# Optimization experiments

Hardware: AMD Instinct MI355X
Metric: run time of the kernel (lower is better)

Reference implementation:

```python
import jax, jax.numpy as jnp
import numpy as np
import math

B, D, L = 32, 128, 512
NH = 8
DK = D // NH  # 16
DV = D // NH  # 16


def setup_inputs() -> dict:
    key = jax.random.key(0)
    kx, kq, kk, kv, ko = jax.random.split(key, 5)
    # xavier_normal std for [B, Dk, D] slabs: gain*sqrt(2/(fan_in+fan_out)) with fan over last two dims
    std_qkv = math.sqrt(2.0 / (DK + D))
    std_o = math.sqrt(2.0 / (DV * NH + D))
    x = jax.random.normal(kx, (B, D, L), dtype=jnp.float32)
    Wqs = jax.random.normal(kq, (NH, B, DK, D), dtype=jnp.float32) * std_qkv
    Wks = jax.random.normal(kk, (NH, B, DK, D), dtype=jnp.float32) * std_qkv
    Wvs = jax.random.normal(kv, (NH, B, DV, D), dtype=jnp.float32) * std_qkv
    Wo = jax.random.normal(ko, (B, DV * NH, D), dtype=jnp.float32) * std_o
    return {"x": x, "Wqs": Wqs, "Wks": Wks, "Wvs": Wvs, "Wo": Wo}


def reference(x, Wqs, Wks, Wvs, Wo):
    # x: [B, D, L]; Wqs/Wks: [NH, B, DK, D]; Wvs: [NH, B, DV, D]; Wo: [B, DV*NH, D]
    nh, b, dk, d = Wqs.shape
    l = x.shape[-1]
    inv_sqrt_dk = 1.0 / math.sqrt(dk)
    Q = jnp.einsum('nbkd,bdl->nbkl', Wqs, x)  # [NH, B, DK, L]
    K = jnp.einsum('nbkd,bdl->nbkl', Wks, x)  # [NH, B, DK, L]
    V = jnp.einsum('nbvd,bdl->nbvl', Wvs, x)  # [NH, B, DV, L]
    # scores[n,b,l,m] = sum_k Q[n,b,k,l]*K[n,b,k,m]; softmax over l (torch dim=1 of [B,L,L])
    scores = jnp.einsum('nbkl,nbkm->nblm', Q, K) * inv_sqrt_dk
    S = jax.nn.softmax(scores, axis=2)
    heads = jnp.einsum('nbvl,nblm->nbvm', V, S)  # [NH, B, DV, L]
    # .pop() in the original reverses head order before concatenation
    heads = heads[::-1]
    head = heads.transpose(1, 0, 2, 3).reshape(b, nh * heads.shape[2], l)  # [B, NH*DV, L]
    out = jnp.einsum('bod,bdl->bol', Wo, head)  # [B, D, L]
    return out
```

## Files before the change

kernel.cpp:

```cpp
#include <hip/hip_runtime.h>
#include <hip/hip_bf16.h>
#include <math.h>

#define B_   32
#define D_   128
#define L_   512
#define NH_  8
#define DK_  16

#define QKS  24
#define VST  520

#define LOG2E 1.4426950408889634f
#define QSC   (0.25f * LOG2E)
#define SH2   (-11.541560327111707f)

typedef _Float16 h2 __attribute__((ext_vector_type(2)));
typedef _Float16 h4 __attribute__((ext_vector_type(4)));
typedef _Float16 h8 __attribute__((ext_vector_type(8)));
typedef __attribute__((ext_vector_type(4)))  float f32x4;
typedef __attribute__((ext_vector_type(16))) float f32x16;
typedef unsigned int u32x2 __attribute__((ext_vector_type(2)));
typedef unsigned int u32x4 __attribute__((ext_vector_type(4)));

__device__ __forceinline__ unsigned int cvt_pk_u(float a, float b) {
    return __builtin_bit_cast(unsigned int, __builtin_amdgcn_cvt_pkrtz(a, b));
}

#define MFMA_K32(a, b, c) __builtin_amdgcn_mfma_f32_16x16x32_f16((a), (b), (c), 0, 0, 0)
#define MFMA_32(a, b, c)  __builtin_amdgcn_mfma_f32_32x32x16_f16((a), (b), (c), 0, 0, 0)

__global__ __launch_bounds__(256) void xcast(
    const float* __restrict__ x,
    _Float16* __restrict__ xt)
{
    __shared__ _Float16 T[64][130];
    const int lt = blockIdx.x;
    const int b  = blockIdx.y;
    const int t  = threadIdx.x;
    const float* xb = x + (size_t)b * D_ * L_;
    _Float16* xtb = xt + (size_t)b * L_ * D_;

    #pragma unroll
    for (int i = t; i < 64 * 128; i += 256) {
        const int l = i & 63, d = i >> 6;
        T[l][d] = (_Float16)xb[(size_t)d * L_ + lt * 64 + l];
    }
    __syncthreads();
    #pragma unroll
    for (int i = t; i < 64 * 128; i += 256) {
        const int d = i & 127, l = i >> 7;
        xtb[(size_t)(lt * 64 + l) * D_ + d] = T[l][d];
    }
}

__global__ __launch_bounds__(512, 2) void attn_mfma(
    const _Float16* __restrict__ xt,
    const float* __restrict__ Wq,
    const float* __restrict__ Wk,
    const float* __restrict__ Wv,
    _Float16* __restrict__ Ht)
{
    __shared__ __attribute__((aligned(16))) _Float16 Qh[512 * QKS];
    __shared__ __attribute__((aligned(16))) _Float16 Kh[512 * QKS];
    __shared__ __attribute__((aligned(16))) _Float16 Vs[32 * VST];

    const int nb = blockIdx.x;
    const int n  = nb >> 5;
    const int b  = nb & 31;
    const int t  = threadIdx.x;
    const int wv = t >> 6;
    const int ln = t & 63;
    const int l16 = ln & 15;
    const int g4  = ln >> 4;
    const int lm  = ln & 31;
    const int hi  = ln >> 5;

    const _Float16* xtb = xt + (size_t)b * L_ * D_;
    const size_t woff = (size_t)(n * B_ + b) * DK_ * D_;
    const float* pWq = Wq + woff;
    const float* pWk = Wk + woff;
    const float* pWv = Wv + woff;

    {
        const h8 ones8 = {(_Float16)1.f,(_Float16)1.f,(_Float16)1.f,(_Float16)1.f,
                          (_Float16)1.f,(_Float16)1.f,(_Float16)1.f,(_Float16)1.f};
        #pragma unroll
        for (int i = 0; i < 2; ++i) {
            const int c = t + i * 512;
            const int row = 16 + (c >> 6), cc = (c & 63) * 8;
            *(h8*)&Vs[row * VST + cc] = ones8;
        }
    }

    f32x4 Qa[4], Ka[4], Va[4];
    #pragma unroll
    for (int lt = 0; lt < 4; ++lt) {
        Qa[lt] = (f32x4){0.f,0.f,0.f,0.f};
        Ka[lt] = (f32x4){0.f,0.f,0.f,0.f};
        Va[lt] = (f32x4){0.f,0.f,0.f,0.f};
    }

    #pragma unroll
    for (int ks = 0; ks < 4; ++ks) {
        const int d0 = ks * 32 + g4 * 8;
        const float* aq = pWq + l16 * D_ + d0;
        const float* ak = pWk + l16 * D_ + d0;
        const float* av = pWv + l16 * D_ + d0;
        const float4 q0 = *(const float4*)aq, q1 = *(const float4*)(aq + 4);
        const float4 k0 = *(const float4*)ak, k1 = *(const float4*)(ak + 4);
        const float4 v0 = *(const float4*)av, v1 = *(const float4*)(av + 4);
        h8 Aq, Ak, Av;
        Aq[0]=(_Float16)q0.x; Aq[1]=(_Float16)q0.y; Aq[2]=(_Float16)q0.z; Aq[3]=(_Float16)q0.w;
        Aq[4]=(_Float16)q1.x; Aq[5]=(_Float16)q1.y; Aq[6]=(_Float16)q1.z; Aq[7]=(_Float16)q1.w;
        Ak[0]=(_Float16)k0.x; Ak[1]=(_Float16)k0.y; Ak[2]=(_Float16)k0.z; Ak[3]=(_Float16)k0.w;
        Ak[4]=(_Float16)k1.x; Ak[5]=(_Float16)k1.y; Ak[6]=(_Float16)k1.z; Ak[7]=(_Float16)k1.w;
        Av[0]=(_Float16)v0.x; Av[1]=(_Float16)v0.y; Av[2]=(_Float16)v0.z; Av[3]=(_Float16)v0.w;
        Av[4]=(_Float16)v1.x; Av[5]=(_Float16)v1.y; Av[6]=(_Float16)v1.z; Av[7]=(_Float16)v1.w;
        #pragma unroll
        for (int lt = 0; lt < 4; ++lt) {
            const int l = wv * 64 + lt * 16 + l16;
            const h8 Bx = *(const h8*)&xtb[(size_t)l * D_ + d0];
            Qa[lt] = MFMA_K32(Aq, Bx, Qa[lt]);
            Ka[lt] = MFMA_K32(Ak, Bx, Ka[lt]);
            Va[lt] = MFMA_K32(Av, Bx, Va[lt]);
        }
    }

    #pragma unroll
    for (int lt = 0; lt < 4; ++lt) {
        const int l = wv * 64 + lt * 16 + l16;
        h4 qv, kv;
        #pragma unroll
        for (int r = 0; r < 4; ++r) {
            qv[r] = (_Float16)(Qa[lt][r] * QSC);
            kv[r] = (_Float16)Ka[lt][r];
            Vs[(g4 * 4 + r) * VST + l] = (_Float16)Va[lt][r];
        }
        *(h4*)&Qh[l * QKS + g4 * 4] = qv;
        *(h4*)&Kh[l * QKS + g4 * 4] = kv;
    }
    __syncthreads();

    const int m0 = wv * 64;
    const h8 Bk0 = *(const h8*)&Kh[(m0 + lm) * QKS + 8 * hi];
    const h8 Bk1 = *(const h8*)&Kh[(m0 + 32 + lm) * QKS + 8 * hi];

    f32x16 shiftacc, pv0, pv1;
    #pragma unroll
    for (int i = 0; i < 16; ++i) { shiftacc[i] = SH2; pv0[i] = 0.f; pv1[i] = 0.f; }

    #pragma unroll 2
    for (int t32 = 0; t32 < 16; ++t32) {
        const int lb = t32 * 32;
        const h8 Aq2 = *(const h8*)&Qh[(lb + lm) * QKS + 8 * hi];
        const h8 Bv1 = *(const h8*)&Vs[lm * VST + lb + 8 * hi];
        const h8 Bv2 = *(const h8*)&Vs[lm * VST + lb + 16 + 8 * hi];

        const f32x16 sc0 = MFMA_32(Aq2, Bk0, shiftacc);
        const f32x16 sc1 = MFMA_32(Aq2, Bk1, shiftacc);

        float pA[16], pB[16];
        #pragma unroll
        for (int r = 0; r < 16; ++r) pA[r] = __builtin_amdgcn_exp2f(sc0[r]);
        #pragma unroll
        for (int r = 0; r < 16; ++r) pB[r] = __builtin_amdgcn_exp2f(sc1[r]);

        const unsigned int a0 = cvt_pk_u(pA[0],  pA[1]);
        const unsigned int a1 = cvt_pk_u(pA[2],  pA[3]);
        const unsigned int a2 = cvt_pk_u(pA[4],  pA[5]);
        const unsigned int a3 = cvt_pk_u(pA[6],  pA[7]);
        const unsigned int a4 = cvt_pk_u(pA[8],  pA[9]);
        const unsigned int a5 = cvt_pk_u(pA[10], pA[11]);
        const unsigned int a6 = cvt_pk_u(pA[12], pA[13]);
        const unsigned int a7 = cvt_pk_u(pA[14], pA[15]);
        const unsigned int b0 = cvt_pk_u(pB[0],  pB[1]);
        const unsigned int b1 = cvt_pk_u(pB[2],  pB[3]);
        const unsigned int b2 = cvt_pk_u(pB[4],  pB[5]);
        const unsigned int b3 = cvt_pk_u(pB[6],  pB[7]);
        const unsigned int b4 = cvt_pk_u(pB[8],  pB[9]);
        const unsigned int b5 = cvt_pk_u(pB[10], pB[11]);
        const unsigned int b6 = cvt_pk_u(pB[12], pB[13]);
        const unsigned int b7 = cvt_pk_u(pB[14], pB[15]);

        const u32x2 sA02 = __builtin_amdgcn_permlane32_swap(a0, a2, false, false);
        const u32x2 sA13 = __builtin_amdgcn_permlane32_swap(a1, a3, false, false);
        const u32x2 sA46 = __builtin_amdgcn_permlane32_swap(a4, a6, false, false);
        const u32x2 sA57 = __builtin_amdgcn_permlane32_swap(a5, a7, false, false);
        const u32x2 sB02 = __builtin_amdgcn_permlane32_swap(b0, b2, false, false);
        const u32x2 sB13 = __builtin_amdgcn_permlane32_swap(b1, b3, false, false);
        const u32x2 sB46 = __builtin_amdgcn_permlane32_swap(b4, b6, false, false);
        const u32x2 sB57 = __builtin_amdgcn_permlane32_swap(b5, b7, false, false);
        const h8 A1m0 = __builtin_bit_cast(h8, (u32x4){sA02.x, sA13.x, sA02.y, sA13.y});
        const h8 A2m0 = __builtin_bit_cast(h8, (u32x4){sA46.x, sA57.x, sA46.y, sA57.y});
        const h8 A1m1 = __builtin_bit_cast(h8, (u32x4){sB02.x, sB13.x, sB02.y, sB13.y});
        const h8 A2m1 = __builtin_bit_cast(h8, (u32x4){sB46.x, sB57.x, sB46.y, sB57.y});

        pv0 = MFMA_32(A1m0, Bv1, pv0);
        pv0 = MFMA_32(A2m0, Bv2, pv0);
        pv1 = MFMA_32(A1m1, Bv1, pv1);
        pv1 = MFMA_32(A2m1, Bv2, pv1);
    }

    const int kk = (NH_ - 1 - n) * 16 + l16;
    const int zlane = 16 + 32 * hi;
    _Float16* Hb = Ht + (size_t)b * 512 * 128;
    #pragma unroll
    for (int r = 0; r < 16; ++r) {
        const int mrow = (r & 3) + 8 * (r >> 2) + 4 * hi;
        const float zr0 = __shfl(pv0[r], zlane);
        const float zr1 = __shfl(pv1[r], zlane);
        const float rz0 = __builtin_amdgcn_rcpf(zr0);
        const float rz1 = __builtin_amdgcn_rcpf(zr1);
        if (lm < 16) {
            Hb[(size_t)(m0 + mrow) * 128 + kk]      = (_Float16)(pv0[r] * rz0);
            Hb[(size_t)(m0 + 32 + mrow) * 128 + kk] = (_Float16)(pv1[r] * rz1);
        }
    }
}

__global__ __launch_bounds__(512) void out_proj_mfma(
    const float* __restrict__ Wo,
    const _Float16* __restrict__ Ht,
    float* __restrict__ out)
{
    const int ct = blockIdx.x;
    const int b  = blockIdx.y;
    const int t  = threadIdx.x;
    const int wv = t >> 6;
    const int ln = t & 63;
    const int l16 = ln & 15;
    const int g4  = ln >> 4;

    const float* Wb = Wo + (size_t)b * D_ * D_;
    const _Float16* Hb = Ht + (size_t)b * 512 * 128;

    f32x4 acc[4];
    #pragma unroll
    for (int nt = 0; nt < 4; ++nt) acc[nt] = (f32x4){0.f,0.f,0.f,0.f};

    #pragma unroll
    for (int ks = 0; ks < 4; ++ks) {
        const int k0 = ks * 32 + g4 * 8;
        const float* ap = Wb + (size_t)(wv * 16 + l16) * D_ + k0;
        const float4 w0 = *(const float4*)ap, w1 = *(const float4*)(ap + 4);
        h8 Ah;
        Ah[0]=(_Float16)w0.x; Ah[1]=(_Float16)w0.y; Ah[2]=(_Float16)w0.z; Ah[3]=(_Float16)w0.w;
        Ah[4]=(_Float16)w1.x; Ah[5]=(_Float16)w1.y; Ah[6]=(_Float16)w1.z; Ah[7]=(_Float16)w1.w;
        #pragma unroll
        for (int nt = 0; nt < 4; ++nt) {
            const h8 Bh = *(const h8*)&Hb[(size_t)(ct * 64 + nt * 16 + l16) * 128 + k0];
            acc[nt] = MFMA_K32(Ah, Bh, acc[nt]);
        }
    }

    float* ob = out + (size_t)b * D_ * L_;
    #pragma unroll
    for (int nt = 0; nt < 4; ++nt) {
        #pragma unroll
        for (int r = 0; r < 4; ++r) {
            ob[(size_t)(wv * 16 + g4 * 4 + r) * L_ + ct * 64 + nt * 16 + l16] = acc[nt][r];
        }
    }
}

extern "C" void kernel_launch(void* const* d_in, const int* in_sizes, int n_in,
                              void* d_out, int out_size, void* d_ws, size_t ws_size,
                              hipStream_t stream)
{
    const float* x  = (const float*)d_in[0];
    const float* Wq = (const float*)d_in[1];
    const float* Wk = (const float*)d_in[2];
    const float* Wv = (const float*)d_in[3];
    const float* Wo = (const float*)d_in[4];
    float* out = (float*)d_out;

    _Float16* Ht = (_Float16*)d_ws;
    _Float16* xt = Ht + (size_t)B_ * 512 * 128;

    xcast<<<dim3(8, B_), dim3(256), 0, stream>>>(x, xt);
    attn_mfma<<<dim3(NH_ * B_), dim3(512), 0, stream>>>(xt, Wq, Wk, Wv, Ht);
    out_proj_mfma<<<dim3(8, B_), dim3(512), 0, stream>>>(Wo, Ht, out);
}
```

Baseline: 40.26 us.

## Fuse x transpose-cast into attention kernel via LDS staging

Removes the separate xcast kernel and instead has each attention block load fp32 x slices, convert to fp16 and transpose into an LDS tile per K-step before the QKV MFMAs. This eliminates one kernel launch and the global round trip of the fp16 transposed x. In exchange, each of the 8 head blocks per batch re-reads and re-converts the same x, adds two barriers per K-step, and raises LDS usage (about 40KB more), which may hurt the two-blocks-per-CU occupancy target.

```diff
diff --git a/kernel.cpp b/kernel.cpp
--- a/kernel.cpp
+++ b/kernel.cpp
@@ -10,6 +10,7 @@
 
 #define QKS  24
 #define VST  520
+#define XST  40
 
 #define LOG2E 1.4426950408889634f
 #define QSC   (0.25f * LOG2E)
@@ -30,37 +31,14 @@
 #define MFMA_K32(a, b, c) __builtin_amdgcn_mfma_f32_16x16x32_f16((a), (b), (c), 0, 0, 0)
 #define MFMA_32(a, b, c)  __builtin_amdgcn_mfma_f32_32x32x16_f16((a), (b), (c), 0, 0, 0)
 
-__global__ __launch_bounds__(256) void xcast(
+__global__ __launch_bounds__(512, 2) void attn_mfma(
     const float* __restrict__ x,
-    _Float16* __restrict__ xt)
-{
-    __shared__ _Float16 T[64][130];
-    const int lt = blockIdx.x;
-    const int b  = blockIdx.y;
-    const int t  = threadIdx.x;
-    const float* xb = x + (size_t)b * D_ * L_;
-    _Float16* xtb = xt + (size_t)b * L_ * D_;
-
-    #pragma unroll
-    for (int i = t; i < 64 * 128; i += 256) {
-        const int l = i & 63, d = i >> 6;
-        T[l][d] = (_Float16)xb[(size_t)d * L_ + lt * 64 + l];
-    }
-    __syncthreads();
-    #pragma unroll
-    for (int i = t; i < 64 * 128; i += 256) {
-        const int d = i & 127, l = i >> 7;
-        xtb[(size_t)(lt * 64 + l) * D_ + d] = T[l][d];
-    }
-}
-
-__global__ __launch_bounds__(512, 2) void attn_mfma(
-    const _Float16* __restrict__ xt,
     const float* __restrict__ Wq,
     const float* __restrict__ Wk,
     const float* __restrict__ Wv,
     _Float16* __restrict__ Ht)
 {
+    __shared__ __attribute__((aligned(16))) _Float16 T32[512 * XST];
     __shared__ __attribute__((aligned(16))) _Float16 Qh[512 * QKS];
     __shared__ __attribute__((aligned(16))) _Float16 Kh[512 * QKS];
     __shared__ __attribute__((aligned(16))) _Float16 Vs[32 * VST];
@@ -76,7 +54,7 @@
     const int lm  = ln & 31;
     const int hi  = ln >> 5;
 
-    const _Float16* xtb = xt + (size_t)b * L_ * D_;
+    const float* xb = x + (size_t)b * D_ * L_;
     const size_t woff = (size_t)(n * B_ + b) * DK_ * D_;
     const float* pWq = Wq + woff;
     const float* pWk = Wk + woff;
@@ -93,6 +71,9 @@
         }
     }
 
+    const int sdd = (t >> 7) * 8;
+    const int sl0 = (t & 127) * 4;
+
     f32x4 Qa[4], Ka[4], Va[4];
     #pragma unroll
     for (int lt = 0; lt < 4; ++lt) {
@@ -101,30 +82,45 @@
         Va[lt] = (f32x4){0.f,0.f,0.f,0.f};
     }
 
-    #pragma unroll
     for (int ks = 0; ks < 4; ++ks) {
+        {
+            f32x4 xv[8];
+            #pragma unroll
+            for (int j = 0; j < 8; ++j)
+                xv[j] = *(const f32x4*)&xb[(size_t)(ks * 32 + sdd + j) * L_ + sl0];
+            #pragma unroll
+            for (int i = 0; i < 4; ++i) {
+                h8 w;
+                #pragma unroll
+                for (int j = 0; j < 8; ++j) w[j] = (_Float16)xv[j][i];
+                *(h8*)&T32[(sl0 + i) * XST + sdd] = w;
+            }
+        }
+        __syncthreads();
+
         const int d0 = ks * 32 + g4 * 8;
         const float* aq = pWq + l16 * D_ + d0;
         const float* ak = pWk + l16 * D_ + d0;
         const float* av = pWv + l16 * D_ + d0;
-        const float4 q0 = *(const float4*)aq, q1 = *(const float4*)(aq + 4);
-        const float4 k0 = *(const float4*)ak, k1 = *(const float4*)(ak + 4);
-        const float4 v0 = *(const float4*)av, v1 = *(const float4*)(av + 4);
+        const f32x4 q0 = *(const f32x4*)aq, q1 = *(const f32x4*)(aq + 4);
+        const f32x4 k0 = *(const f32x4*)ak, k1 = *(const f32x4*)(ak + 4);
+        const f32x4 v0 = *(const f32x4*)av, v1 = *(const f32x4*)(av + 4);
         h8 Aq, Ak, Av;
-        Aq[0]=(_Float16)q0.x; Aq[1]=(_Float16)q0.y; Aq[2]=(_Float16)q0.z; Aq[3]=(_Float16)q0.w;
-        Aq[4]=(_Float16)q1.x; Aq[5]=(_Float16)q1.y; Aq[6]=(_Float16)q1.z; Aq[7]=(_Float16)q1.w;
-        Ak[0]=(_Float16)k0.x; Ak[1]=(_Float16)k0.y; Ak[2]=(_Float16)k0.z; Ak[3]=(_Float16)k0.w;
-        Ak[4]=(_Float16)k1.x; Ak[5]=(_Float16)k1.y; Ak[6]=(_Float16)k1.z; Ak[7]=(_Float16)k1.w;
-        Av[0]=(_Float16)v0.x; Av[1]=(_Float16)v0.y; Av[2]=(_Float16)v0.z; Av[3]=(_Float16)v0.w;
-        Av[4]=(_Float16)v1.x; Av[5]=(_Float16)v1.y; Av[6]=(_Float16)v1.z; Av[7]=(_Float16)v1.w;
+        #pragma unroll
+        for (int j = 0; j < 4; ++j) {
+            Aq[j] = (_Float16)q0[j]; Aq[j + 4] = (_Float16)q1[j];
+            Ak[j] = (_Float16)k0[j]; Ak[j + 4] = (_Float16)k1[j];
+            Av[j] = (_Float16)v0[j]; Av[j + 4] = (_Float16)v1[j];
+        }
         #pragma unroll
         for (int lt = 0; lt < 4; ++lt) {
             const int l = wv * 64 + lt * 16 + l16;
-            const h8 Bx = *(const h8*)&xtb[(size_t)l * D_ + d0];
+            const h8 Bx = *(const h8*)&T32[l * XST + g4 * 8];
             Qa[lt] = MFMA_K32(Aq, Bx, Qa[lt]);
             Ka[lt] = MFMA_K32(Ak, Bx, Ka[lt]);
             Va[lt] = MFMA_K32(Av, Bx, Va[lt]);
         }
+        __syncthreads();
     }
 
     #pragma unroll
@@ -243,10 +239,12 @@
     for (int ks = 0; ks < 4; ++ks) {
         const int k0 = ks * 32 + g4 * 8;
         const float* ap = Wb + (size_t)(wv * 16 + l16) * D_ + k0;
-        const float4 w0 = *(const float4*)ap, w1 = *(const float4*)(ap + 4);
+        const f32x4 w0 = *(const f32x4*)ap, w1 = *(const f32x4*)(ap + 4);
         h8 Ah;
-        Ah[0]=(_Float16)w0.x; Ah[1]=(_Float16)w0.y; Ah[2]=(_Float16)w0.z; Ah[3]=(_Float16)w0.w;
-        Ah[4]=(_Float16)w1.x; Ah[5]=(_Float16)w1.y; Ah[6]=(_Float16)w1.z; Ah[7]=(_Float16)w1.w;
+        #pragma unroll
+        for (int j = 0; j < 4; ++j) {
+            Ah[j] = (_Float16)w0[j]; Ah[j + 4] = (_Float16)w1[j];
+        }
         #pragma unroll
         for (int nt = 0; nt < 4; ++nt) {
             const h8 Bh = *(const h8*)&Hb[(size_t)(ct * 64 + nt * 16 + l16) * 128 + k0];
@@ -276,9 +274,7 @@
     float* out = (float*)d_out;
 
     _Float16* Ht = (_Float16*)d_ws;
-    _Float16* xt = Ht + (size_t)B_ * 512 * 128;
-
-    xcast<<<dim3(8, B_), dim3(256), 0, stream>>>(x, xt);
-    attn_mfma<<<dim3(NH_ * B_), dim3(512), 0, stream>>>(xt, Wq, Wk, Wv, Ht);
+
+    attn_mfma<<<dim3(NH_ * B_), dim3(512), 0, stream>>>(x, Wq, Wk, Wv, Ht);
     out_proj_mfma<<<dim3(8, B_), dim3(512), 0, stream>>>(Wo, Ht, out);
 }
```

Result: faster. 34.95 us (-13.2%).
